# Performance work log

Measured on AMD Instinct MI355X. Metric: run time of the kernel, lower is better.

The kernel has to match this reference:

```python
import jax, jax.numpy as jnp
import numpy as np

N_SUB = 60000   # nodes in current subgraph (rows of fnode/agraph/subnode)
M = 120000      # total messages (directed edges)
K = 8           # max neighbors per node/message
H = 128         # hidden_size
IN = 256        # input_size (fmess feature dim)
FD = 128        # node_fdim
DEPTH = 2       # rnn depth (sparse_forward iterations)
NUM_NODES = 65536


def setup_inputs() -> dict:
    key = jax.random.key(0)
    ks = jax.random.split(key, 12)
    s = 0.05
    def w(k, shape):
        return jax.random.normal(k, shape, jnp.float32) * s
    return {
        "fnode": jax.random.normal(ks[0], (N_SUB, FD), jnp.float32),
        "fmess": jax.random.normal(ks[1], (M, IN), jnp.float32),
        "agraph": jax.random.randint(ks[2], (N_SUB, K), 0, M, dtype=jnp.int32),
        "bgraph": jax.random.randint(ks[3], (M, K), 0, M, dtype=jnp.int32),
        "h_in": jax.random.normal(ks[4], (M, H), jnp.float32),
        "c_in": jax.random.normal(ks[5], (M, H), jnp.float32),
        "submess": jnp.arange(N_SUB, dtype=jnp.int32),
        "subnode": jnp.arange(N_SUB, dtype=jnp.int32),
        "num_nodes": NUM_NODES,
        # tree-LSTM gate weights, stored [in_dim, out_dim]
        "Wi": w(ks[6], (IN + H, H)), "bi": jnp.zeros((H,), jnp.float32),
        "Wo": w(ks[7], (IN + H, H)), "bo": jnp.zeros((H,), jnp.float32),
        "Wf": w(ks[8], (IN + H, H)), "bf": jnp.zeros((H,), jnp.float32),
        "Wu": w(ks[9], (IN + H, H)), "bu": jnp.zeros((H,), jnp.float32),
        # node readout W_o: Linear(node_fdim + hidden -> hidden) + ReLU (+ Dropout = eval no-op)
        "Wn": w(ks[10], (FD + H, H)), "bn": jnp.zeros((H,), jnp.float32),
    }


def _lstm_cell(x, h_nei, c_nei, Wi, bi, Wo, bo, Wf, bf, Wu, bu):
    # x: [S, IN]; h_nei, c_nei: [S, K, H]  (hgraph-style child-sum tree LSTM)
    h_sum = h_nei.sum(axis=1)                         # [S, H]
    z = jnp.concatenate([x, h_sum], axis=-1)          # [S, IN+H]
    i = jax.nn.sigmoid(z @ Wi + bi)
    o = jax.nn.sigmoid(z @ Wo + bo)
    u = jnp.tanh(z @ Wu + bu)
    # per-neighbor forget gate: sigmoid(cat([x_expand, h_nei]) @ Wf + bf),
    # split the matmul so we never materialize the [S, K, IN+H] concat
    d_in = x.shape[1]
    fx = x @ Wf[:d_in] + bf                           # [S, H]
    f = jax.nn.sigmoid(fx[:, None, :] + h_nei @ Wf[d_in:])  # [S, K, H]
    c = i * u + (f * c_nei).sum(axis=1)
    h = o * jnp.tanh(c)
    return h, c


def reference(fnode, fmess, agraph, bgraph, h_in, c_in, submess, subnode, num_nodes,
              Wi, bi, Wo, bo, Wf, bf, Wu, bu, Wn, bn):
    # LSTM.sparse_forward: zero state at submess rows, then iteratively update them
    mask = jnp.ones((h_in.shape[0],), h_in.dtype).at[submess].set(0.0)
    h = h_in * mask[:, None]
    c = c_in * mask[:, None]
    x_sub = fmess[submess]       # [S, IN]
    bg_sub = bgraph[submess]     # [S, K] message-neighbor ids
    for _ in range(DEPTH):
        h_nei = h[bg_sub]        # [S, K, H] gather
        c_nei = c[bg_sub]
        sub_h, sub_c = _lstm_cell(x_sub, h_nei, c_nei, Wi, bi, Wo, bo, Wf, bf, Wu, bu)
        h = h.at[submess].set(sub_h)   # index_scatter
        c = c.at[submess].set(sub_c)
    # node update: gather incoming messages, sum, Linear + ReLU (dropout inactive at eval)
    nei_message = h[agraph].sum(axis=1)                      # [N_SUB, H]
    node_hiddens = jnp.concatenate([fnode, nei_message], axis=-1)
    node_hiddens = jax.nn.relu(node_hiddens @ Wn + bn)       # [N_SUB, H]
    node_buf = jnp.zeros((num_nodes, node_hiddens.shape[1]), node_hiddens.dtype)
    node_buf = node_buf.at[subnode].set(node_hiddens)        # index_scatter into full buffer
    return node_buf, h, c
```

## Files before the change

### kernel.cpp

```cpp
#include <hip/hip_runtime.h>
#include <cstdint>
#include <cstddef>

#define Hc   128
#define INc  256
#define Kc   8
#define HP   136
#define HSP  136
#define EPH  136
#define ZP2  264
#define XOP  520
#define HCS  384

typedef unsigned short ushortT;
typedef __attribute__((ext_vector_type(8))) short bf16x8;
typedef __attribute__((ext_vector_type(4))) float f32x4;
typedef __attribute__((ext_vector_type(4))) unsigned short us4;
typedef __attribute__((ext_vector_type(8))) unsigned short us8;

__device__ __forceinline__ float fsig(float x) {
  return __builtin_amdgcn_rcpf(1.f + __expf(-x));
}
__device__ __forceinline__ float ftanh(float x) {
  float e = __expf(2.f * fminf(x, 15.f));
  return (e - 1.f) * __builtin_amdgcn_rcpf(e + 1.f);
}
__device__ __forceinline__ ushortT f2bf(float f) {
  unsigned u = __builtin_bit_cast(unsigned, f);
  unsigned r = (u + 0x7fffu + ((u >> 16) & 1u)) >> 16;
  return (ushortT)r;
}
__device__ __forceinline__ us4 f2bf4(float4 v) {
  us4 o; o[0] = f2bf(v.x); o[1] = f2bf(v.y); o[2] = f2bf(v.z); o[3] = f2bf(v.w);
  return o;
}
__device__ __forceinline__ us8 f2bf8(float4 a, float4 b) {
  us8 o;
  o[0] = f2bf(a.x); o[1] = f2bf(a.y); o[2] = f2bf(a.z); o[3] = f2bf(a.w);
  o[4] = f2bf(b.x); o[5] = f2bf(b.y); o[6] = f2bf(b.z); o[7] = f2bf(b.w);
  return o;
}
__device__ __forceinline__ float bf2f(ushortT u) {
  return __builtin_bit_cast(float, (unsigned)u << 16);
}

#define GATE_FRAGS (4*8*12*64)
#define WN_FRAGS   (8*8*64)

__global__ void marks_init(int* __restrict__ mark, int M, int* __restrict__ nmark, int NN) {
  int i = blockIdx.x * blockDim.x + threadIdx.x;
  if (i < M) mark[i] = -1;
  if (i < NN) nmark[i] = -1;
}

__global__ void set_repack(const int* __restrict__ submess, const int* __restrict__ subnode,
                           int S, int* __restrict__ mark, int* __restrict__ nmark,
                           const float* __restrict__ Wi, const float* __restrict__ Wo,
                           const float* __restrict__ Wu, const float* __restrict__ Wf,
                           const float* __restrict__ Wn, ushortT* __restrict__ pack, int SB) {
  if ((int)blockIdx.x < SB) {
    int i = blockIdx.x * 256 + threadIdx.x;
    if (i < S) { mark[submess[i]] = i; nmark[subnode[i]] = i; }
    return;
  }
  int idx = (blockIdx.x - SB) * 256 + threadIdx.x;
  if (idx < GATE_FRAGS) {
    int lane = idx & 63;
    int kt = (idx >> 6) % 12;
    int gc = idx / (64 * 12);
    int c = gc & 7, g = gc >> 3;
    const float* W = (g == 0) ? Wi : (g == 1) ? Wo : (g == 2) ? Wu : Wf;
    int k0 = kt * 32 + (lane >> 4) * 8;
    int col = c * 16 + (lane & 15);
    ushortT* dst = pack + (size_t)idx * 8;
    #pragma unroll
    for (int j = 0; j < 8; ++j) dst[j] = f2bf(W[(size_t)(k0 + j) * Hc + col]);
  } else if (idx < GATE_FRAGS + WN_FRAGS) {
    int i2 = idx - GATE_FRAGS;
    int lane = i2 & 63;
    int kt = (i2 >> 6) & 7;
    int c = i2 >> 9;
    int k0 = kt * 32 + (lane >> 4) * 8;
    int col = c * 16 + (lane & 15);
    ushortT* dst = pack + (size_t)GATE_FRAGS * 8 + (size_t)i2 * 8;
    #pragma unroll
    for (int j = 0; j < 8; ++j) dst[j] = f2bf(Wn[(size_t)(k0 + j) * Hc + col]);
  }
}

__device__ __forceinline__ const bf16x8* wh_frag(const ushortT* pack, int g, int cw, int kf, int lane) {
  return (const bf16x8*)&pack[(size_t)(((g * 8 + cw) * 12 + (8 + kf)) * 64 + lane) * 8];
}

__global__ __launch_bounds__(256) void xg_stage_hf(
    const float* __restrict__ fmess, const int* __restrict__ submess,
    const ushortT* __restrict__ pack,
    const float* __restrict__ bi, const float* __restrict__ bo,
    const float* __restrict__ bu, const float* __restrict__ bfb,
    ushortT* __restrict__ Xg,
    const float* __restrict__ h_in, const float* __restrict__ c_in,
    const int* __restrict__ mark,
    float* __restrict__ h_out, float* __restrict__ c_out,
    ushortT* __restrict__ HCF,
    int M, int S, int XB)
{
  __shared__ __align__(16) ushortT xs[32 * ZP2];
  __shared__ int aux[32];
  const int t = threadIdx.x;
  const int w = t >> 6, lane = t & 63, lg = lane >> 4, cl = lane & 15;

  if ((int)blockIdx.x < XB) {
    const int row0 = blockIdx.x * 32;
    if (t < 32) aux[t] = (row0 + t < S) ? submess[row0 + t] : -1;
    __syncthreads();
    #pragma unroll
    for (int rr = 0; rr < 2; ++rr) {
      int r = (t >> 4) + rr * 16, cp = t & 15;
      int ms = aux[r];
      const float4* xr = (ms >= 0) ? (const float4*)(fmess + (size_t)ms * INc) : nullptr;
      #pragma unroll
      for (int q = 0; q < 4; ++q) {
        int slot = cp + q * 16;
        float4 v;
        if (xr) v = xr[slot]; else { v.x = v.y = v.z = v.w = 0.f; }
        *(us4*)&xs[r * ZP2 + slot * 4] = f2bf4(v);
      }
    }
    __syncthreads();

    f32x4 acc0[8], acc1[8];
    #pragma unroll
    for (int i = 0; i < 8; ++i) {
      acc0[i] = (f32x4){0.f, 0.f, 0.f, 0.f};
      acc1[i] = (f32x4){0.f, 0.f, 0.f, 0.f};
    }
    const ushortT* zrA = &xs[cl * ZP2 + lg * 8];
    const ushortT* zrB = &xs[(16 + cl) * ZP2 + lg * 8];
    #pragma unroll
    for (int kt = 0; kt < 8; ++kt) {
      bf16x8 a0 = *(const bf16x8*)&zrA[kt * 32];
      bf16x8 a1 = *(const bf16x8*)&zrB[kt * 32];
      #pragma unroll
      for (int c = 0; c < 8; ++c) {
        bf16x8 b = *(const bf16x8*)&pack[(size_t)(((w * 8 + c) * 12 + kt) * 64 + lane) * 8];
        acc0[c] = __builtin_amdgcn_mfma_f32_16x16x32_bf16(a0, b, acc0[c], 0, 0, 0);
        acc1[c] = __builtin_amdgcn_mfma_f32_16x16x32_bf16(a1, b, acc1[c], 0, 0, 0);
      }
    }
    __syncthreads();
    const float* bias = (w == 0) ? bi : (w == 1) ? bo : (w == 2) ? bu : bfb;
    #pragma unroll
    for (int mt = 0; mt < 2; ++mt) {
      #pragma unroll
      for (int c = 0; c < 8; ++c) {
        int col = c * 16 + cl;
        float bv = bias[col];
        #pragma unroll
        for (int reg = 0; reg < 4; ++reg) {
          float v = (mt ? acc1[c][reg] : acc0[c][reg]) + bv;
          xs[(lg * 4 + reg) * XOP + w * 128 + col] = f2bf(v);
        }
      }
      __syncthreads();
      {
        int r = t >> 4, cc = t & 15;
        int s = row0 + mt * 16 + r;
        if (s < S) {
          const ushortT* src = &xs[r * XOP + cc * 32];
          ushortT* dst = &Xg[(size_t)s * 512 + cc * 32];
          *(us8*)&dst[0]  = *(const us8*)&src[0];
          *(us8*)&dst[8]  = *(const us8*)&src[8];
          *(us8*)&dst[16] = *(const us8*)&src[16];
          *(us8*)&dst[24] = *(const us8*)&src[24];
        }
      }
      __syncthreads();
    }
    return;
  }

  ushortT* zh = xs;
  int* mk = aux;
  const int row0 = (blockIdx.x - XB) * 16;

  if (blockIdx.x == XB && t < 48) {
    us8 z;
    #pragma unroll
    for (int e = 0; e < 8; ++e) z[e] = 0;
    *(us8*)&HCF[(size_t)(M + S) * HCS + t * 8] = z;
  }
  if (t < 16) mk[t] = (row0 + t < M) ? mark[row0 + t] : 0;
  __syncthreads();
  {
    int r = t >> 4, cp = t & 15;
    int j = row0 + r;
    us8 hz;
    #pragma unroll
    for (int e = 0; e < 8; ++e) hz[e] = 0;
    if (j < M && mk[r] < 0) {
      const float4* h4 = (const float4*)(h_in + (size_t)j * Hc);
      const float4* c4 = (const float4*)(c_in + (size_t)j * Hc);
      float4 a0 = h4[cp * 2], a1 = h4[cp * 2 + 1];
      float4 b0 = c4[cp * 2], b1 = c4[cp * 2 + 1];
      ((float4*)(h_out + (size_t)j * Hc))[cp * 2] = a0;
      ((float4*)(h_out + (size_t)j * Hc))[cp * 2 + 1] = a1;
      ((float4*)(c_out + (size_t)j * Hc))[cp * 2] = b0;
      ((float4*)(c_out + (size_t)j * Hc))[cp * 2 + 1] = b1;
      us8 h8 = f2bf8(a0, a1);
      *(us8*)&HCF[(size_t)j * HCS + cp * 8] = h8;
      *(us8*)&HCF[(size_t)j * HCS + 128 + cp * 8] = f2bf8(b0, b1);
      hz = h8;
    }
    *(us8*)&zh[r * HP + cp * 8] = hz;
  }
  __syncthreads();

  f32x4 acc0 = (f32x4){0.f,0.f,0.f,0.f}, acc1 = acc0;
  const ushortT* zr = &zh[cl * HP + lg * 8];
  #pragma unroll
  for (int kf = 0; kf < 4; ++kf) {
    bf16x8 a = *(const bf16x8*)&zr[kf * 32];
    acc0 = __builtin_amdgcn_mfma_f32_16x16x32_bf16(a, *wh_frag(pack, 3, w*2+0, kf, lane), acc0, 0, 0, 0);
    acc1 = __builtin_amdgcn_mfma_f32_16x16x32_bf16(a, *wh_frag(pack, 3, w*2+1, kf, lane), acc1, 0, 0, 0);
  }
  __syncthreads();
  #pragma unroll
  for (int half = 0; half < 2; ++half) {
    int col = (w * 2 + half) * 16 + cl;
    f32x4 a_ = half ? acc1 : acc0;
    #pragma unroll
    for (int reg = 0; reg < 4; ++reg)
      zh[(lg * 4 + reg) * HP + col] = f2bf(a_[reg]);
  }
  __syncthreads();
  {
    int r = t >> 4, cp = t & 15;
    if (row0 + r < M && mk[r] < 0)
      *(us8*)&HCF[(size_t)(row0 + r) * HCS + 256 + cp * 8] = *(const us8*)&zh[r * HP + cp * 8];
  }
}

template<int MODE>
__global__ __launch_bounds__(256) void lstm8(
    const int* __restrict__ submess, const int* __restrict__ bgraph,
    const int* __restrict__ mark,
    ushortT* HCF,
    const ushortT* __restrict__ Xg, const ushortT* __restrict__ pack,
    ushortT* hsumNS, ushortT* cpartNS,
    float* __restrict__ dstH, float* __restrict__ dstC, int S, int M)
{
  __shared__ __align__(16) ushortT zs[16 * HSP];
  __shared__ __align__(16) ushortT pih[16 * EPH];
  __shared__ __align__(16) ushortT poh[16 * EPH];
  __shared__ __align__(16) ushortT puh[16 * EPH];
  __shared__ int nbj[16][Kc];
  __shared__ int msrow[16];

  const int t = threadIdx.x;
  const int row0 = blockIdx.x * 16;
  const int DUMMY = M + S;

  if (t < 128) {
    int r = t >> 3, k = t & 7;
    int s = row0 + r;
    int ms = (s < S) ? submess[s] : -1;
    if (k == 0) msrow[r] = ms;
    int j = DUMMY;
    if (ms >= 0) {
      int jj = bgraph[(size_t)ms * Kc + k];
      int m = mark[jj];
      j = (MODE == 0) ? (m >= 0 ? DUMMY : jj) : (m >= 0 ? M + m : DUMMY);
    }
    nbj[r][k] = j;
  }
  __syncthreads();

  {
    int r = t >> 4, cp = t & 15;
    int spos = row0 + r;
    float sum[8] = {0.f,0.f,0.f,0.f,0.f,0.f,0.f,0.f};
    if (MODE == 1 && spos < S) {
      us8 hs = *(const us8*)&hsumNS[(size_t)spos * Hc + cp * 8];
      #pragma unroll
      for (int e = 0; e < 8; ++e) sum[e] = bf2f(hs[e]);
    }
    #pragma unroll
    for (int k = 0; k < Kc; ++k) {
      int j = nbj[r][k];
      us8 v = *(const us8*)&HCF[(size_t)j * HCS + cp * 8];
      #pragma unroll
      for (int e = 0; e < 8; ++e) sum[e] += bf2f(v[e]);
    }
    us8 o8;
    #pragma unroll
    for (int e = 0; e < 8; ++e) o8[e] = f2bf(sum[e]);
    *(us8*)&zs[r * HSP + cp * 8] = o8;
    if (MODE == 0 && spos < S)
      *(us8*)&hsumNS[(size_t)spos * Hc + cp * 8] = o8;
  }
  __syncthreads();

  const int w = t >> 6, lane = t & 63, lg = lane >> 4, cl = lane & 15;

  f32x4 acc[6];
  #pragma unroll
  for (int i = 0; i < 6; ++i) acc[i] = (f32x4){0.f, 0.f, 0.f, 0.f};
  const ushortT* zrow = &zs[cl * HSP + lg * 8];
  #pragma unroll
  for (int kf = 0; kf < 4; ++kf) {
    bf16x8 a = *(const bf16x8*)&zrow[kf * 32];
    #pragma unroll
    for (int g = 0; g < 3; ++g)
      #pragma unroll
      for (int half = 0; half < 2; ++half)
        acc[g * 2 + half] = __builtin_amdgcn_mfma_f32_16x16x32_bf16(
            a, *wh_frag(pack, g, w * 2 + half, kf, lane), acc[g * 2 + half], 0, 0, 0);
  }

  #pragma unroll
  for (int half = 0; half < 2; ++half) {
    int col = (w * 2 + half) * 16 + cl;
    #pragma unroll
    for (int reg = 0; reg < 4; ++reg) {
      int row = lg * 4 + reg;
      pih[row * EPH + col] = f2bf(acc[0 + half][reg]);
      poh[row * EPH + col] = f2bf(acc[2 + half][reg]);
      puh[row * EPH + col] = f2bf(acc[4 + half][reg]);
    }
  }
  __syncthreads();

  {
    int r = t >> 4, cc = t & 15;
    int ms = msrow[r];
    int spos = row0 + r;
    const ushortT* xgr = Xg + (size_t)spos * 512 + cc * 8;
    us8 xi8 = *(const us8*)&xgr[0];
    us8 xo8 = *(const us8*)&xgr[128];
    us8 xu8 = *(const us8*)&xgr[256];
    us8 xf8 = *(const us8*)&xgr[384];
    us8 pi8 = *(const us8*)&pih[r * EPH + cc * 8];
    us8 po8 = *(const us8*)&poh[r * EPH + cc * 8];
    us8 pu8 = *(const us8*)&puh[r * EPH + cc * 8];
    float fx[8], ovv[8], iu[8], cn[8];
    #pragma unroll
    for (int e = 0; e < 8; ++e) {
      float iv = fsig(bf2f(xi8[e]) + bf2f(pi8[e]));
      float uv = ftanh(bf2f(xu8[e]) + bf2f(pu8[e]));
      ovv[e] = fsig(bf2f(xo8[e]) + bf2f(po8[e]));
      fx[e] = bf2f(xf8[e]);
      iu[e] = iv * uv;
      cn[e] = 0.f;
    }
    #pragma unroll
    for (int k = 0; k < Kc; ++k) {
      int j = nbj[r][k];
      us8 hf8 = *(const us8*)&HCF[(size_t)j * HCS + 256 + cc * 8];
      us8 cn8 = *(const us8*)&HCF[(size_t)j * HCS + 128 + cc * 8];
      #pragma unroll
      for (int e = 0; e < 8; ++e)
        cn[e] = fmaf(fsig(fx[e] + bf2f(hf8[e])), bf2f(cn8[e]), cn[e]);
    }
    float cacc[8];
    if (MODE == 1 && spos < S) {
      us8 cp8 = *(const us8*)&cpartNS[(size_t)spos * Hc + cc * 8];
      #pragma unroll
      for (int e = 0; e < 8; ++e) cacc[e] = iu[e] + cn[e] + bf2f(cp8[e]);
    } else {
      #pragma unroll
      for (int e = 0; e < 8; ++e) cacc[e] = iu[e] + cn[e];
    }
    float hv[8];
    #pragma unroll
    for (int e = 0; e < 8; ++e) hv[e] = ovv[e] * ftanh(cacc[e]);

    if (MODE == 0) {
      us8 h8, c8, cn16;
      #pragma unroll
      for (int e = 0; e < 8; ++e) {
        h8[e] = (spos < S) ? f2bf(hv[e]) : (ushortT)0;
        c8[e] = f2bf(cacc[e]);
        cn16[e] = f2bf(cn[e]);
      }
      if (spos < S) {
        *(us8*)&HCF[(size_t)(M + spos) * HCS + cc * 8] = h8;
        *(us8*)&HCF[(size_t)(M + spos) * HCS + 128 + cc * 8] = c8;
        *(us8*)&cpartNS[(size_t)spos * Hc + cc * 8] = cn16;
      }
      *(us8*)&zs[r * HSP + cc * 8] = h8;
    } else {
      if (ms >= 0) {
        float* dh = dstH + (size_t)ms * Hc + cc * 8;
        float* dc = dstC + (size_t)ms * Hc + cc * 8;
        *(float4*)&dh[0] = *(float4*)&hv[0];
        *(float4*)&dh[4] = *(float4*)&hv[4];
        *(float4*)&dc[0] = *(float4*)&cacc[0];
        *(float4*)&dc[4] = *(float4*)&cacc[4];
      }
    }
  }

  if (MODE == 0) {
    __syncthreads();
    f32x4 a0 = (f32x4){0.f,0.f,0.f,0.f}, a1 = a0;
    const ushortT* zr2 = &zs[cl * HSP + lg * 8];
    #pragma unroll
    for (int kf = 0; kf < 4; ++kf) {
      bf16x8 a = *(const bf16x8*)&zr2[kf * 32];
      a0 = __builtin_amdgcn_mfma_f32_16x16x32_bf16(a, *wh_frag(pack, 3, w*2+0, kf, lane), a0, 0, 0, 0);
      a1 = __builtin_amdgcn_mfma_f32_16x16x32_bf16(a, *wh_frag(pack, 3, w*2+1, kf, lane), a1, 0, 0, 0);
    }
    #pragma unroll
    for (int half = 0; half < 2; ++half) {
      int col = (w * 2 + half) * 16 + cl;
      f32x4 a_ = half ? a1 : a0;
      #pragma unroll
      for (int reg = 0; reg < 4; ++reg)
        pih[(lg * 4 + reg) * EPH + col] = f2bf(a_[reg]);
    }
    __syncthreads();
    {
      int r = t >> 4, cp = t & 15;
      int sp = row0 + r;
      if (sp < S)
        *(us8*)&HCF[(size_t)(M + sp) * HCS + 256 + cp * 8] = *(const us8*)&pih[r * EPH + cp * 8];
    }
  }
}

__global__ __launch_bounds__(256) void readout_zero(
    const float* __restrict__ fnode, const int* __restrict__ agraph,
    const int* __restrict__ subnode, const float* __restrict__ h_out,
    const ushortT* __restrict__ HCF, const int* __restrict__ mark,
    const int* __restrict__ nmark,
    const ushortT* __restrict__ packWn, const float* __restrict__ bn,
    float* __restrict__ node_buf, int Nsub, int num_nodes, int NB, int ZB)
{
  __shared__ __align__(16) ushortT z2[16 * ZP2];
  __shared__ int orow[16];
  __shared__ int jn[16][Kc];

  const int t = threadIdx.x;

  if ((int)blockIdx.x >= NB) {
    long total = (long)num_nodes * 16;
    float4 z; z.x = z.y = z.z = z.w = 0.f;
    for (long idx = (long)(blockIdx.x - NB) * 256 + t; idx < total; idx += (long)ZB * 256) {
      long v = idx >> 4;
      int cp = (int)(idx & 15);
      if (nmark[v] < 0) {
        ((float4*)(node_buf + (size_t)v * Hc))[cp * 2] = z;
        ((float4*)(node_buf + (size_t)v * Hc))[cp * 2 + 1] = z;
      }
    }
    return;
  }

  const int row0 = blockIdx.x * 16;
  if (t < 16) orow[t] = (row0 + t < Nsub) ? subnode[row0 + t] : -1;
  if (t >= 64 && t < 64 + 128) {
    int i = t - 64, r = i >> 3, k = i & 7;
    int v = row0 + r;
    int j = 0;
    if (v < Nsub) {
      j = agraph[(size_t)v * Kc + k];
      if (mark[j] >= 0) j = ~j;
    }
    jn[r][k] = j;
  }
  {
    int r = t >> 4, cp = t & 15;
    int v = row0 + r;
    const float4* fr = (v < Nsub) ? (const float4*)(fnode + (size_t)v * Hc) : nullptr;
    float4 v0, v1; v0.x = v0.y = v0.z = v0.w = 0.f; v1 = v0;
    if (fr) { v0 = fr[cp]; v1 = fr[cp + 16]; }
    *(us4*)&z2[r * ZP2 + cp * 4] = f2bf4(v0);
    *(us4*)&z2[r * ZP2 + 64 + cp * 4] = f2bf4(v1);
  }
  __syncthreads();
  {
    int r = t >> 4, cp = t & 15;
    float sum[8] = {0.f,0.f,0.f,0.f,0.f,0.f,0.f,0.f};
    #pragma unroll
    for (int k = 0; k < Kc; ++k) {
      int je = jn[r][k];
      if (je < 0) {
        int j = ~je;
        float4 p0 = ((const float4*)(h_out + (size_t)j * Hc))[cp * 2];
        float4 p1 = ((const float4*)(h_out + (size_t)j * Hc))[cp * 2 + 1];
        sum[0] += p0.x; sum[1] += p0.y; sum[2] += p0.z; sum[3] += p0.w;
        sum[4] += p1.x; sum[5] += p1.y; sum[6] += p1.z; sum[7] += p1.w;
      } else {
        us8 v = *(const us8*)&HCF[(size_t)je * HCS + cp * 8];
        #pragma unroll
        for (int e = 0; e < 8; ++e) sum[e] += bf2f(v[e]);
      }
    }
    us8 o8;
    #pragma unroll
    for (int e = 0; e < 8; ++e) o8[e] = f2bf(sum[e]);
    *(us8*)&z2[r * ZP2 + Hc + cp * 8] = o8;
  }
  __syncthreads();

  const int w = t >> 6, lane = t & 63;
  const int lg = lane >> 4, cl = lane & 15;

  f32x4 acc0 = (f32x4){0.f,0.f,0.f,0.f};
  f32x4 acc1 = (f32x4){0.f,0.f,0.f,0.f};
  const ushortT* zr = &z2[cl * ZP2 + lg * 8];
  #pragma unroll
  for (int kt = 0; kt < 8; ++kt) {
    bf16x8 a = *(const bf16x8*)&zr[kt * 32];
    bf16x8 b0 = *(const bf16x8*)&packWn[(size_t)(((w * 2 + 0) * 8 + kt) * 64 + lane) * 8];
    bf16x8 b1 = *(const bf16x8*)&packWn[(size_t)(((w * 2 + 1) * 8 + kt) * 64 + lane) * 8];
    acc0 = __builtin_amdgcn_mfma_f32_16x16x32_bf16(a, b0, acc0, 0, 0, 0);
    acc1 = __builtin_amdgcn_mfma_f32_16x16x32_bf16(a, b1, acc1, 0, 0, 0);
  }
  __syncthreads();
  float* zf = (float*)z2;
  #pragma unroll
  for (int half = 0; half < 2; ++half) {
    int col = (w * 2 + half) * 16 + cl;
    float bnv = bn[col];
    f32x4 a_ = half ? acc1 : acc0;
    #pragma unroll
    for (int reg = 0; reg < 4; ++reg)
      zf[(lg * 4 + reg) * 132 + col] = fmaxf(a_[reg] + bnv, 0.f);
  }
  __syncthreads();
  {
    int r = t >> 4, cc = t & 15;
    int o = orow[r];
    if (o >= 0) {
      float* dst = node_buf + (size_t)o * Hc + cc * 8;
      *(float4*)&dst[0] = *(const float4*)&zf[r * 132 + cc * 8];
      *(float4*)&dst[4] = *(const float4*)&zf[r * 132 + cc * 8 + 4];
    }
  }
}

extern "C" void kernel_launch(void* const* d_in, const int* in_sizes, int n_in,
                              void* d_out, int out_size, void* d_ws, size_t ws_size,
                              hipStream_t stream) {
  const float* fnode   = (const float*)d_in[0];
  const float* fmess   = (const float*)d_in[1];
  const int*   agraph  = (const int*)d_in[2];
  const int*   bgraph  = (const int*)d_in[3];
  const float* h_in    = (const float*)d_in[4];
  const float* c_in    = (const float*)d_in[5];
  const int*   submess = (const int*)d_in[6];
  const int*   subnode = (const int*)d_in[7];
  const float* Wi = (const float*)d_in[9];
  const float* bi = (const float*)d_in[10];
  const float* Wo = (const float*)d_in[11];
  const float* bo = (const float*)d_in[12];
  const float* Wf = (const float*)d_in[13];
  const float* bf_ = (const float*)d_in[14];
  const float* Wu = (const float*)d_in[15];
  const float* bu = (const float*)d_in[16];
  const float* Wn = (const float*)d_in[17];
  const float* bn = (const float*)d_in[18];

  const int S    = in_sizes[6];
  const int Nsub = in_sizes[2] / Kc;
  const int M    = in_sizes[4] / Hc;
  const int num_nodes = out_size / Hc - 2 * M;

  float* node_buf = (float*)d_out;
  float* h_out = node_buf + (size_t)num_nodes * Hc;
  float* c_out = h_out + (size_t)M * Hc;

  const int lblocks = (S + 15) / 16;

  int* mark = (int*)d_ws;
  size_t off = (((size_t)M * sizeof(int)) + 255) & ~(size_t)255;
  int* nmark = (int*)((char*)d_ws + off);
  off += (((size_t)num_nodes * sizeof(int)) + 255) & ~(size_t)255;
  ushortT* pack = (ushortT*)((char*)d_ws + off);
  off += (((size_t)(GATE_FRAGS + WN_FRAGS) * 8 * sizeof(ushortT)) + 255) & ~(size_t)255;
  ushortT* HCF = (ushortT*)((char*)d_ws + off);
  off += (((size_t)(M + S + 1) * HCS * sizeof(ushortT)) + 255) & ~(size_t)255;
  ushortT* Xg = (ushortT*)((char*)d_ws + off);
  ushortT* packWn = pack + (size_t)GATE_FRAGS * 8;
  ushortT* cpartNS = (ushortT*)node_buf;
  ushortT* hsumNS  = cpartNS + (size_t)S * Hc;

  int initN = (M > num_nodes) ? M : num_nodes;
  hipLaunchKernelGGL(marks_init, dim3((initN + 255) / 256), dim3(256), 0, stream,
                     mark, M, nmark, num_nodes);
  {
    int SB = (S + 255) / 256;
    int RB = (GATE_FRAGS + WN_FRAGS + 255) / 256;
    hipLaunchKernelGGL(set_repack, dim3(SB + RB), dim3(256), 0, stream,
                       submess, subnode, S, mark, nmark, Wi, Wo, Wu, Wf, Wn, pack, SB);
  }
  {
    int XB = (S + 31) / 32;
    int SB2 = (M + 15) / 16;
    hipLaunchKernelGGL(xg_stage_hf, dim3(XB + SB2), dim3(256), 0, stream,
                       fmess, submess, pack, bi, bo, bu, bf_, Xg,
                       h_in, c_in, mark, h_out, c_out, HCF,
                       M, S, XB);
  }
  hipLaunchKernelGGL(lstm8<0>, dim3(lblocks), dim3(256), 0, stream,
      submess, bgraph, mark, HCF, Xg, pack,
      hsumNS, cpartNS, h_out, c_out, S, M);
  hipLaunchKernelGGL(lstm8<1>, dim3(lblocks), dim3(256), 0, stream,
      submess, bgraph, mark, HCF, Xg, pack,
      hsumNS, cpartNS, h_out, c_out, S, M);
  {
    int NB = (Nsub + 15) / 16;
    int ZB = 512;
    hipLaunchKernelGGL(readout_zero, dim3(NB + ZB), dim3(256), 0, stream,
        fnode, agraph, subnode, h_out, HCF, mark, nmark, packWn, bn,
        node_buf, Nsub, num_nodes, NB, ZB);
  }
}
```

Baseline: 276.6 us.

## Fuse x-gate GEMM into LSTM kernels and use nontemporal output stores

The separate precomputation of the x-projection gates (stored as a 512-wide bf16 Xg buffer) is removed. The staging kernel now only converts the gathered fmess rows to a bf16 X16 buffer. Each LSTM depth kernel recomputes x@W for all four gates with MFMA and adds the biases in its epilogue. Separately, nontemporal stores are used for h/c copies, c outputs, and the node_buf writes. This trades a smaller intermediate buffer (256 instead of 512 bf16 per row) for doing the x-gate GEMM twice, once per depth, plus extra LDS use.

```diff
diff --git a/kernel.cpp b/kernel.cpp
--- a/kernel.cpp
+++ b/kernel.cpp
@@ -9,7 +9,6 @@
 #define HSP  136
 #define EPH  136
 #define ZP2  264
-#define XOP  520
 #define HCS  384
 
 typedef unsigned short ushortT;
@@ -17,6 +16,10 @@
 typedef __attribute__((ext_vector_type(4))) float f32x4;
 typedef __attribute__((ext_vector_type(4))) unsigned short us4;
 typedef __attribute__((ext_vector_type(8))) unsigned short us8;
+
+__device__ __forceinline__ void nt_store4(const float* src, float* dst) {
+  __builtin_nontemporal_store(*(const f32x4*)src, (f32x4*)dst);
+}
 
 __device__ __forceinline__ float fsig(float x) {
   return __builtin_amdgcn_rcpf(1.f + __expf(-x));
@@ -88,171 +91,120 @@
   }
 }
 
+__device__ __forceinline__ const bf16x8* g_frag(const ushortT* pack, int g, int cw, int kt, int lane) {
+  return (const bf16x8*)&pack[(size_t)(((g * 8 + cw) * 12 + kt) * 64 + lane) * 8];
+}
 __device__ __forceinline__ const bf16x8* wh_frag(const ushortT* pack, int g, int cw, int kf, int lane) {
   return (const bf16x8*)&pack[(size_t)(((g * 8 + cw) * 12 + (8 + kf)) * 64 + lane) * 8];
 }
 
-__global__ __launch_bounds__(256) void xg_stage_hf(
-    const float* __restrict__ fmess, const int* __restrict__ submess,
-    const ushortT* __restrict__ pack,
-    const float* __restrict__ bi, const float* __restrict__ bo,
-    const float* __restrict__ bu, const float* __restrict__ bfb,
-    ushortT* __restrict__ Xg,
+__global__ __launch_bounds__(256) void stage_hf_xconv(
     const float* __restrict__ h_in, const float* __restrict__ c_in,
     const int* __restrict__ mark,
     float* __restrict__ h_out, float* __restrict__ c_out,
     ushortT* __restrict__ HCF,
-    int M, int S, int XB)
+    const float* __restrict__ fmess, const int* __restrict__ submess,
+    ushortT* __restrict__ X16,
+    const ushortT* __restrict__ pack, int M, int S, int SB)
 {
-  __shared__ __align__(16) ushortT xs[32 * ZP2];
-  __shared__ int aux[32];
+  __shared__ __align__(16) ushortT zh[16 * HP];
+  __shared__ int aux[16];
   const int t = threadIdx.x;
   const int w = t >> 6, lane = t & 63, lg = lane >> 4, cl = lane & 15;
 
-  if ((int)blockIdx.x < XB) {
-    const int row0 = blockIdx.x * 32;
-    if (t < 32) aux[t] = (row0 + t < S) ? submess[row0 + t] : -1;
+  if ((int)blockIdx.x < SB) {
+    const int row0 = blockIdx.x * 16;
+    if (blockIdx.x == 0 && t < 48) {
+      us8 z;
+      #pragma unroll
+      for (int e = 0; e < 8; ++e) z[e] = 0;
+      *(us8*)&HCF[(size_t)(M + S) * HCS + t * 8] = z;
+    }
+    if (t < 16) aux[t] = (row0 + t < M) ? mark[row0 + t] : 0;
     __syncthreads();
-    #pragma unroll
-    for (int rr = 0; rr < 2; ++rr) {
-      int r = (t >> 4) + rr * 16, cp = t & 15;
-      int ms = aux[r];
-      const float4* xr = (ms >= 0) ? (const float4*)(fmess + (size_t)ms * INc) : nullptr;
-      #pragma unroll
-      for (int q = 0; q < 4; ++q) {
-        int slot = cp + q * 16;
-        float4 v;
-        if (xr) v = xr[slot]; else { v.x = v.y = v.z = v.w = 0.f; }
-        *(us4*)&xs[r * ZP2 + slot * 4] = f2bf4(v);
+    {
+      int r = t >> 4, cp = t & 15;
+      int j = row0 + r;
+      us8 hz;
+      #pragma unroll
+      for (int e = 0; e < 8; ++e) hz[e] = 0;
+      if (j < M && aux[r] < 0) {
+        const float4* h4 = (const float4*)(h_in + (size_t)j * Hc);
+        const float4* c4 = (const float4*)(c_in + (size_t)j * Hc);
+        float4 a0 = h4[cp * 2], a1 = h4[cp * 2 + 1];
+        float4 b0 = c4[cp * 2], b1 = c4[cp * 2 + 1];
+        nt_store4(&a0.x, h_out + (size_t)j * Hc + cp * 8);
+        nt_store4(&a1.x, h_out + (size_t)j * Hc + cp * 8 + 4);
+        nt_store4(&b0.x, c_out + (size_t)j * Hc + cp * 8);
+        nt_store4(&b1.x, c_out + (size_t)j * Hc + cp * 8 + 4);
+        us8 h8 = f2bf8(a0, a1);
+        *(us8*)&HCF[(size_t)j * HCS + cp * 8] = h8;
+        *(us8*)&HCF[(size_t)j * HCS + 128 + cp * 8] = f2bf8(b0, b1);
+        hz = h8;
       }
+      *(us8*)&zh[r * HP + cp * 8] = hz;
     }
     __syncthreads();
 
-    f32x4 acc0[8], acc1[8];
-    #pragma unroll
-    for (int i = 0; i < 8; ++i) {
-      acc0[i] = (f32x4){0.f, 0.f, 0.f, 0.f};
-      acc1[i] = (f32x4){0.f, 0.f, 0.f, 0.f};
-    }
-    const ushortT* zrA = &xs[cl * ZP2 + lg * 8];
-    const ushortT* zrB = &xs[(16 + cl) * ZP2 + lg * 8];
-    #pragma unroll
-    for (int kt = 0; kt < 8; ++kt) {
-      bf16x8 a0 = *(const bf16x8*)&zrA[kt * 32];
-      bf16x8 a1 = *(const bf16x8*)&zrB[kt * 32];
-      #pragma unroll
-      for (int c = 0; c < 8; ++c) {
-        bf16x8 b = *(const bf16x8*)&pack[(size_t)(((w * 8 + c) * 12 + kt) * 64 + lane) * 8];
-        acc0[c] = __builtin_amdgcn_mfma_f32_16x16x32_bf16(a0, b, acc0[c], 0, 0, 0);
-        acc1[c] = __builtin_amdgcn_mfma_f32_16x16x32_bf16(a1, b, acc1[c], 0, 0, 0);
-      }
+    f32x4 acc0 = (f32x4){0.f,0.f,0.f,0.f}, acc1 = acc0;
+    const ushortT* zr = &zh[cl * HP + lg * 8];
+    #pragma unroll
+    for (int kf = 0; kf < 4; ++kf) {
+      bf16x8 a = *(const bf16x8*)&zr[kf * 32];
+      acc0 = __builtin_amdgcn_mfma_f32_16x16x32_bf16(a, *wh_frag(pack, 3, w*2+0, kf, lane), acc0, 0, 0, 0);
+      acc1 = __builtin_amdgcn_mfma_f32_16x16x32_bf16(a, *wh_frag(pack, 3, w*2+1, kf, lane), acc1, 0, 0, 0);
     }
     __syncthreads();
-    const float* bias = (w == 0) ? bi : (w == 1) ? bo : (w == 2) ? bu : bfb;
-    #pragma unroll
-    for (int mt = 0; mt < 2; ++mt) {
-      #pragma unroll
-      for (int c = 0; c < 8; ++c) {
-        int col = c * 16 + cl;
-        float bv = bias[col];
-        #pragma unroll
-        for (int reg = 0; reg < 4; ++reg) {
-          float v = (mt ? acc1[c][reg] : acc0[c][reg]) + bv;
-          xs[(lg * 4 + reg) * XOP + w * 128 + col] = f2bf(v);
-        }
-      }
-      __syncthreads();
-      {
-        int r = t >> 4, cc = t & 15;
-        int s = row0 + mt * 16 + r;
-        if (s < S) {
-          const ushortT* src = &xs[r * XOP + cc * 32];
-          ushortT* dst = &Xg[(size_t)s * 512 + cc * 32];
-          *(us8*)&dst[0]  = *(const us8*)&src[0];
-          *(us8*)&dst[8]  = *(const us8*)&src[8];
-          *(us8*)&dst[16] = *(const us8*)&src[16];
-          *(us8*)&dst[24] = *(const us8*)&src[24];
-        }
-      }
-      __syncthreads();
+    #pragma unroll
+    for (int half = 0; half < 2; ++half) {
+      int col = (w * 2 + half) * 16 + cl;
+      f32x4 a_ = half ? acc1 : acc0;
+      #pragma unroll
+      for (int reg = 0; reg < 4; ++reg)
+        zh[(lg * 4 + reg) * HP + col] = f2bf(a_[reg]);
+    }
+    __syncthreads();
+    {
+      int r = t >> 4, cp = t & 15;
+      if (row0 + r < M && aux[r] < 0)
+        *(us8*)&HCF[(size_t)(row0 + r) * HCS + 256 + cp * 8] = *(const us8*)&zh[r * HP + cp * 8];
     }
     return;
   }
 
-  ushortT* zh = xs;
-  int* mk = aux;
-  const int row0 = (blockIdx.x - XB) * 16;
-
-  if (blockIdx.x == XB && t < 48) {
-    us8 z;
-    #pragma unroll
-    for (int e = 0; e < 8; ++e) z[e] = 0;
-    *(us8*)&HCF[(size_t)(M + S) * HCS + t * 8] = z;
-  }
-  if (t < 16) mk[t] = (row0 + t < M) ? mark[row0 + t] : 0;
+  const int row0 = (blockIdx.x - SB) * 16;
+  if (t < 16) aux[t] = (row0 + t < S) ? submess[row0 + t] : -1;
   __syncthreads();
   {
     int r = t >> 4, cp = t & 15;
-    int j = row0 + r;
-    us8 hz;
-    #pragma unroll
-    for (int e = 0; e < 8; ++e) hz[e] = 0;
-    if (j < M && mk[r] < 0) {
-      const float4* h4 = (const float4*)(h_in + (size_t)j * Hc);
-      const float4* c4 = (const float4*)(c_in + (size_t)j * Hc);
-      float4 a0 = h4[cp * 2], a1 = h4[cp * 2 + 1];
-      float4 b0 = c4[cp * 2], b1 = c4[cp * 2 + 1];
-      ((float4*)(h_out + (size_t)j * Hc))[cp * 2] = a0;
-      ((float4*)(h_out + (size_t)j * Hc))[cp * 2 + 1] = a1;
-      ((float4*)(c_out + (size_t)j * Hc))[cp * 2] = b0;
-      ((float4*)(c_out + (size_t)j * Hc))[cp * 2 + 1] = b1;
-      us8 h8 = f2bf8(a0, a1);
-      *(us8*)&HCF[(size_t)j * HCS + cp * 8] = h8;
-      *(us8*)&HCF[(size_t)j * HCS + 128 + cp * 8] = f2bf8(b0, b1);
-      hz = h8;
-    }
-    *(us8*)&zh[r * HP + cp * 8] = hz;
-  }
-  __syncthreads();
-
-  f32x4 acc0 = (f32x4){0.f,0.f,0.f,0.f}, acc1 = acc0;
-  const ushortT* zr = &zh[cl * HP + lg * 8];
-  #pragma unroll
-  for (int kf = 0; kf < 4; ++kf) {
-    bf16x8 a = *(const bf16x8*)&zr[kf * 32];
-    acc0 = __builtin_amdgcn_mfma_f32_16x16x32_bf16(a, *wh_frag(pack, 3, w*2+0, kf, lane), acc0, 0, 0, 0);
-    acc1 = __builtin_amdgcn_mfma_f32_16x16x32_bf16(a, *wh_frag(pack, 3, w*2+1, kf, lane), acc1, 0, 0, 0);
-  }
-  __syncthreads();
-  #pragma unroll
-  for (int half = 0; half < 2; ++half) {
-    int col = (w * 2 + half) * 16 + cl;
-    f32x4 a_ = half ? acc1 : acc0;
-    #pragma unroll
-    for (int reg = 0; reg < 4; ++reg)
-      zh[(lg * 4 + reg) * HP + col] = f2bf(a_[reg]);
-  }
-  __syncthreads();
-  {
-    int r = t >> 4, cp = t & 15;
-    if (row0 + r < M && mk[r] < 0)
-      *(us8*)&HCF[(size_t)(row0 + r) * HCS + 256 + cp * 8] = *(const us8*)&zh[r * HP + cp * 8];
+    int s = row0 + r;
+    int ms = aux[r];
+    if (ms >= 0) {
+      const float4* xr = (const float4*)(fmess + (size_t)ms * INc + cp * 16);
+      float4 v0 = xr[0], v1 = xr[1], v2 = xr[2], v3 = xr[3];
+      *(us8*)&X16[(size_t)s * INc + cp * 16] = f2bf8(v0, v1);
+      *(us8*)&X16[(size_t)s * INc + cp * 16 + 8] = f2bf8(v2, v3);
+    }
   }
 }
 
 template<int MODE>
-__global__ __launch_bounds__(256) void lstm8(
+__global__ __launch_bounds__(256) void lstm9(
     const int* __restrict__ submess, const int* __restrict__ bgraph,
     const int* __restrict__ mark,
-    ushortT* HCF,
-    const ushortT* __restrict__ Xg, const ushortT* __restrict__ pack,
+    ushortT* HCF, const ushortT* __restrict__ X16,
+    const ushortT* __restrict__ pack,
+    const float* __restrict__ bi, const float* __restrict__ bo,
+    const float* __restrict__ bu, const float* __restrict__ bfb,
     ushortT* hsumNS, ushortT* cpartNS,
     float* __restrict__ dstH, float* __restrict__ dstC, int S, int M)
 {
   __shared__ __align__(16) ushortT zs[16 * HSP];
+  __shared__ __align__(16) ushortT xs[16 * ZP2];
   __shared__ __align__(16) ushortT pih[16 * EPH];
   __shared__ __align__(16) ushortT poh[16 * EPH];
   __shared__ __align__(16) ushortT puh[16 * EPH];
+  __shared__ __align__(16) ushortT pfh[16 * EPH];
   __shared__ int nbj[16][Kc];
   __shared__ int msrow[16];
 
@@ -278,6 +230,12 @@
   {
     int r = t >> 4, cp = t & 15;
     int spos = row0 + r;
+    {
+      size_t sidx = (size_t)((spos < S) ? spos : 0) * INc + cp * 16;
+      const us8* xr = (const us8*)&X16[sidx];
+      *(us8*)&xs[r * ZP2 + cp * 16] = xr[0];
+      *(us8*)&xs[r * ZP2 + cp * 16 + 8] = xr[1];
+    }
     float sum[8] = {0.f,0.f,0.f,0.f,0.f,0.f,0.f,0.f};
     if (MODE == 1 && spos < S) {
       us8 hs = *(const us8*)&hsumNS[(size_t)spos * Hc + cp * 8];
@@ -302,19 +260,30 @@
 
   const int w = t >> 6, lane = t & 63, lg = lane >> 4, cl = lane & 15;
 
-  f32x4 acc[6];
+  f32x4 acc[8];
   #pragma unroll
-  for (int i = 0; i < 6; ++i) acc[i] = (f32x4){0.f, 0.f, 0.f, 0.f};
+  for (int i = 0; i < 8; ++i) acc[i] = (f32x4){0.f, 0.f, 0.f, 0.f};
+  const ushortT* xrow = &xs[cl * ZP2 + lg * 8];
   const ushortT* zrow = &zs[cl * HSP + lg * 8];
+  #pragma unroll
+  for (int kt = 0; kt < 8; ++kt) {
+    bf16x8 a = *(const bf16x8*)&xrow[kt * 32];
+    #pragma unroll
+    for (int tix = 0; tix < 8; ++tix) {
+      int g = tix >> 1, cw = w * 2 + (tix & 1);
+      acc[tix] = __builtin_amdgcn_mfma_f32_16x16x32_bf16(
+          a, *g_frag(pack, g, cw, kt, lane), acc[tix], 0, 0, 0);
+    }
+  }
   #pragma unroll
   for (int kf = 0; kf < 4; ++kf) {
     bf16x8 a = *(const bf16x8*)&zrow[kf * 32];
     #pragma unroll
-    for (int g = 0; g < 3; ++g)
-      #pragma unroll
-      for (int half = 0; half < 2; ++half)
-        acc[g * 2 + half] = __builtin_amdgcn_mfma_f32_16x16x32_bf16(
-            a, *wh_frag(pack, g, w * 2 + half, kf, lane), acc[g * 2 + half], 0, 0, 0);
+    for (int tix = 0; tix < 6; ++tix) {
+      int g = tix >> 1, cw = w * 2 + (tix & 1);
+      acc[tix] = __builtin_amdgcn_mfma_f32_16x16x32_bf16(
+          a, *wh_frag(pack, g, cw, kf, lane), acc[tix], 0, 0, 0);
+    }
   }
 
   #pragma unroll
@@ -326,6 +295,7 @@
       pih[row * EPH + col] = f2bf(acc[0 + half][reg]);
       poh[row * EPH + col] = f2bf(acc[2 + half][reg]);
       puh[row * EPH + col] = f2bf(acc[4 + half][reg]);
+      pfh[row * EPH + col] = f2bf(acc[6 + half][reg]);
     }
   }
   __syncthreads();
@@ -334,21 +304,28 @@
     int r = t >> 4, cc = t & 15;
     int ms = msrow[r];
     int spos = row0 + r;
-    const ushortT* xgr = Xg + (size_t)spos * 512 + cc * 8;
-    us8 xi8 = *(const us8*)&xgr[0];
-    us8 xo8 = *(const us8*)&xgr[128];
-    us8 xu8 = *(const us8*)&xgr[256];
-    us8 xf8 = *(const us8*)&xgr[384];
     us8 pi8 = *(const us8*)&pih[r * EPH + cc * 8];
     us8 po8 = *(const us8*)&poh[r * EPH + cc * 8];
     us8 pu8 = *(const us8*)&puh[r * EPH + cc * 8];
+    us8 pf8 = *(const us8*)&pfh[r * EPH + cc * 8];
+    float bia[8], boa[8], bua[8], bfa[8];
+    {
+      *(float4*)&bia[0] = ((const float4*)(bi + cc * 8))[0];
+      *(float4*)&bia[4] = ((const float4*)(bi + cc * 8))[1];
+      *(float4*)&boa[0] = ((const float4*)(bo + cc * 8))[0];
+      *(float4*)&boa[4] = ((const float4*)(bo + cc * 8))[1];
+      *(float4*)&bua[0] = ((const float4*)(bu + cc * 8))[0];
+      *(float4*)&bua[4] = ((const float4*)(bu + cc * 8))[1];
+      *(float4*)&bfa[0] = ((const float4*)(bfb + cc * 8))[0];
+      *(float4*)&bfa[4] = ((const float4*)(bfb + cc * 8))[1];
+    }
     float fx[8], ovv[8], iu[8], cn[8];
     #pragma unroll
     for (int e = 0; e < 8; ++e) {
-      float iv = fsig(bf2f(xi8[e]) + bf2f(pi8[e]));
-      float uv = ftanh(bf2f(xu8[e]) + bf2f(pu8[e]));
-      ovv[e] = fsig(bf2f(xo8[e]) + bf2f(po8[e]));
-      fx[e] = bf2f(xf8[e]);
+      float iv = fsig(bf2f(pi8[e]) + bia[e]);
+      float uv = ftanh(bf2f(pu8[e]) + bua[e]);
+      ovv[e] = fsig(bf2f(po8[e]) + boa[e]);
+      fx[e] = bf2f(pf8[e]) + bfa[e];
       iu[e] = iv * uv;
       cn[e] = 0.f;
     }
@@ -394,8 +371,8 @@
         float* dc = dstC + (size_t)ms * Hc + cc * 8;
         *(float4*)&dh[0] = *(float4*)&hv[0];
         *(float4*)&dh[4] = *(float4*)&hv[4];
-        *(float4*)&dc[0] = *(float4*)&cacc[0];
-        *(float4*)&dc[4] = *(float4*)&cacc[4];
+        nt_store4(&cacc[0], &dc[0]);
+        nt_store4(&cacc[4], &dc[4]);
       }
     }
   }
@@ -444,13 +421,13 @@
 
   if ((int)blockIdx.x >= NB) {
     long total = (long)num_nodes * 16;
-    float4 z; z.x = z.y = z.z = z.w = 0.f;
+    float zbuf[4] = {0.f, 0.f, 0.f, 0.f};
     for (long idx = (long)(blockIdx.x - NB) * 256 + t; idx < total; idx += (long)ZB * 256) {
       long v = idx >> 4;
       int cp = (int)(idx & 15);
       if (nmark[v] < 0) {
-        ((float4*)(node_buf + (size_t)v * Hc))[cp * 2] = z;
-        ((float4*)(node_buf + (size_t)v * Hc))[cp * 2 + 1] = z;
+        nt_store4(zbuf, node_buf + (size_t)v * Hc + cp * 8);
+        nt_store4(zbuf, node_buf + (size_t)v * Hc + cp * 8 + 4);
       }
     }
     return;
@@ -534,8 +511,8 @@
     int o = orow[r];
     if (o >= 0) {
       float* dst = node_buf + (size_t)o * Hc + cc * 8;
-      *(float4*)&dst[0] = *(const float4*)&zf[r * 132 + cc * 8];
-      *(float4*)&dst[4] = *(const float4*)&zf[r * 132 + cc * 8 + 4];
+      nt_store4(&zf[r * 132 + cc * 8], &dst[0]);
+      nt_store4(&zf[r * 132 + cc * 8 + 4], &dst[4]);
     }
   }
 }
@@ -581,7 +558,7 @@
   off += (((size_t)(GATE_FRAGS + WN_FRAGS) * 8 * sizeof(ushortT)) + 255) & ~(size_t)255;
   ushortT* HCF = (ushortT*)((char*)d_ws + off);
   off += (((size_t)(M + S + 1) * HCS * sizeof(ushortT)) + 255) & ~(size_t)255;
-  ushortT* Xg = (ushortT*)((char*)d_ws + off);
+  ushortT* X16 = (ushortT*)((char*)d_ws + off);
   ushortT* packWn = pack + (size_t)GATE_FRAGS * 8;
   ushortT* cpartNS = (ushortT*)node_buf;
   ushortT* hsumNS  = cpartNS + (size_t)S * Hc;
@@ -596,18 +573,16 @@
                        submess, subnode, S, mark, nmark, Wi, Wo, Wu, Wf, Wn, pack, SB);
   }
   {
-    int XB = (S + 31) / 32;
     int SB2 = (M + 15) / 16;
-    hipLaunchKernelGGL(xg_stage_hf, dim3(XB + SB2), dim3(256), 0, stream,
-                       fmess, submess, pack, bi, bo, bu, bf_, Xg,
+    hipLaunchKernelGGL(stage_hf_xconv, dim3(SB2 + lblocks), dim3(256), 0, stream,
                        h_in, c_in, mark, h_out, c_out, HCF,
-                       M, S, XB);
-  }
-  hipLaunchKernelGGL(lstm8<0>, dim3(lblocks), dim3(256), 0, stream,
-      submess, bgraph, mark, HCF, Xg, pack,
+                       fmess, submess, X16, pack, M, S, SB2);
+  }
+  hipLaunchKernelGGL(lstm9<0>, dim3(lblocks), dim3(256), 0, stream,
+      submess, bgraph, mark, HCF, X16, pack, bi, bo, bu, bf_,
       hsumNS, cpartNS, h_out, c_out, S, M);
-  hipLaunchKernelGGL(lstm8<1>, dim3(lblocks), dim3(256), 0, stream,
-      submess, bgraph, mark, HCF, Xg, pack,
+  hipLaunchKernelGGL(lstm9<1>, dim3(lblocks), dim3(256), 0, stream,
+      submess, bgraph, mark, HCF, X16, pack, bi, bo, bu, bf_,
       hsumNS, cpartNS, h_out, c_out, S, M);
   {
     int NB = (Nsub + 15) / 16;
```

Result: slower. 290.3 us (+5.0%).
